# Optimization experiments

Hardware: AMD Instinct MI355X
Metric: run time of the kernel (lower is better)

The kernel has to match this reference:

```python
import jax, jax.numpy as jnp
import numpy as np

N, E, F_IN, F_OUT = 16384, 4096, 128, 128
EPS = 1e-6


def setup_inputs() -> dict:
    key = jax.random.key(0)
    k1, k2, k3 = jax.random.split(key, 3)
    H = (jax.random.uniform(k1, (N, E)) < 0.05).astype(jnp.float32)
    x = jax.random.normal(k2, (N, F_IN), dtype=jnp.float32)
    W = jax.random.normal(k3, (F_IN, F_OUT), dtype=jnp.float32) * 0.05
    return {"x": x, "H": H, "W": W}


def reference(x, H, W):
    # D_v^{-1} H D_e^{-1} H^T x W, computed without materializing the NxN
    # adjacency: diagonal matmuls become row/col broadcast scaling, and the
    # GEMM chain is reordered right-to-left (same math, associativity).
    d_e_inv = 1.0 / (H.sum(axis=0) + EPS)   # [E]
    d_v_inv = 1.0 / (H.sum(axis=1) + EPS)   # [N]
    xw = x @ W                               # [N, F_out]
    edge_msg = H.T @ xw                      # [E, F_out] gather onto edges
    edge_msg = d_e_inv[:, None] * edge_msg   # D_e^{-1}
    node_msg = H @ edge_msg                  # [N, F_out] scatter back to nodes
    return d_v_inv[:, None] * node_msg       # D_v^{-1}
```

## Files before the change

### kernel.cpp

```cpp
#include <hip/hip_runtime.h>
#include <stdint.h>

#define N_NODES 16384
#define N_EDGES 4096
#define FDIM    128
#define EPSF    1e-6f

typedef __attribute__((ext_vector_type(8))) short short8;
typedef __attribute__((ext_vector_type(4))) float f32x4;
typedef unsigned long long ull;

__device__ __forceinline__ unsigned short f2bf(float f) {
    uint32_t u = __float_as_uint(f);
    return (unsigned short)((u + 0x7FFFu + ((u >> 16) & 1u)) >> 16);
}
__device__ __forceinline__ short8 as_s8(uint4 v) {
    union { uint4 a; short8 b; } u; u.a = v; return u.b;
}

__device__ __forceinline__ short8 expand8(uint32_t half, int bitoff) {
    uint32_t b8 = (half >> bitoff) & 0xFFu;
    uint32_t lo = ((b8 & 0xFu) * 0x00204081u) & 0x01010101u;
    uint32_t hi = ((b8 >> 4) * 0x00204081u) & 0x01010101u;
    union { short8 v; uint32_t u[4]; } a;
#if __has_builtin(__builtin_amdgcn_perm)
    a.u[0] = __builtin_amdgcn_perm(0u, lo, 0x04010400u) * 0x3F80u;
    a.u[1] = __builtin_amdgcn_perm(0u, lo, 0x04030402u) * 0x3F80u;
    a.u[2] = __builtin_amdgcn_perm(0u, hi, 0x04010400u) * 0x3F80u;
    a.u[3] = __builtin_amdgcn_perm(0u, hi, 0x04030402u) * 0x3F80u;
#else
    a.u[0] = ((lo & 1u)         | ((lo >> 8) & 1u) << 16) * 0x3F80u;
    a.u[1] = (((lo >> 16) & 1u) | ((lo >> 24) & 1u) << 16) * 0x3F80u;
    a.u[2] = ((hi & 1u)         | ((hi >> 8) & 1u) << 16) * 0x3F80u;
    a.u[3] = (((hi >> 16) & 1u) | ((hi >> 24) & 1u) << 16) * 0x3F80u;
#endif
    return a.v;
}

__device__ __forceinline__ ull bit_transpose64(ull q, int lane) {
    const ull M32 = 0xFFFFFFFF00000000ull, M16 = 0xFFFF0000FFFF0000ull,
              M8 = 0xFF00FF00FF00FF00ull, M4 = 0xF0F0F0F0F0F0F0F0ull,
              M2 = 0xCCCCCCCCCCCCCCCCull, M1 = 0xAAAAAAAAAAAAAAAAull;
#define TSTEP(d, Md) { ull tv = __shfl_xor(q, d, 64); \
    q = ((lane & d) == 0) ? ((q & ~Md) | ((tv << d) & Md)) \
                          : ((q & Md) | ((tv >> d) & ~Md)); }
    TSTEP(32, M32) TSTEP(16, M16) TSTEP(8, M8) TSTEP(4, M4) TSTEP(2, M2) TSTEP(1, M1)
#undef TSTEP
    return q;
}

__global__ __launch_bounds__(256) void k_bitpack(const float* __restrict__ H,
        ull* __restrict__ bitsNE, float* __restrict__ dvinv) {
    int w = threadIdx.x >> 6, lane = threadIdx.x & 63;
    int n = blockIdx.x * 4 + w;
    const float4* hr = (const float4*)(H + (size_t)n * N_EDGES);
    ull* out = bitsNE + (size_t)n * (N_EDGES / 64);
    int cnt = 0;
    for (int c4 = 0; c4 < N_EDGES / 256; ++c4) {
        float4 v = hr[c4 * 64 + lane];
        ull b0 = __ballot(v.x > 0.5f);
        ull b1 = __ballot(v.y > 0.5f);
        ull b2 = __ballot(v.z > 0.5f);
        ull b3 = __ballot(v.w > 0.5f);
        cnt += __popcll(b0) + __popcll(b1) + __popcll(b2) + __popcll(b3);
        if (lane == 0) {
            #pragma unroll
            for (int q = 0; q < 4; ++q) {
                ull wq = ((b0 >> (16 * q)) & 0xFFFFull)
                       | (((b1 >> (16 * q)) & 0xFFFFull) << 16)
                       | (((b2 >> (16 * q)) & 0xFFFFull) << 32)
                       | (((b3 >> (16 * q)) & 0xFFFFull) << 48);
                out[c4 * 4 + q] = wq;
            }
        }
    }
    if (lane == 0) dvinv[n] = 1.0f / ((float)cnt + EPSF);
}

__global__ __launch_bounds__(256) void k_transpose_bf(const ull* __restrict__ bitsNE,
        ull* __restrict__ bitsEN) {
    int w = threadIdx.x >> 6, lane = threadIdx.x & 63;
    int wid = blockIdx.x * 4 + w;
    int nt = wid >> 3, etg = wid & 7;
    int pl = 4 * (lane & 15) + (lane >> 4);
    const ull* src = bitsNE + (size_t)(nt * 64 + pl) * (N_EDGES / 64);
    #pragma unroll
    for (int i = 0; i < 8; ++i) {
        int et = etg * 8 + i;
        ull q = src[et];
        q = bit_transpose64(q, lane);
        bitsEN[(size_t)(et * 64 + pl) * (N_NODES / 64) + nt] = q;
    }
}

__global__ __launch_bounds__(256) void k_edeg(const ull* __restrict__ bitsEN,
        float* __restrict__ deinv) {
    int w = threadIdx.x >> 6, lane = threadIdx.x & 63;
    int e = blockIdx.x * 4 + w;
    const ull* r = bitsEN + (size_t)e * (N_NODES / 64);
    int s = __popcll(r[lane]) + __popcll(r[lane + 64]) + __popcll(r[lane + 128]) + __popcll(r[lane + 192]);
    for (int o = 32; o; o >>= 1) s += __shfl_xor(s, o);
    if (lane == 0) deinv[e] = 1.0f / ((float)s + EPSF);
}

__global__ __launch_bounds__(256) void k_xw(const float* __restrict__ x, const float* __restrict__ W,
        unsigned short* __restrict__ xwTp) {
    __shared__ __attribute__((aligned(16))) unsigned short ldsWT[128 * 136];
    __shared__ __attribute__((aligned(16))) unsigned short ldsT[128 * 72];
    int t = threadIdx.x, lane = t & 63, w = t >> 6;
    int r16 = lane & 15, klane = lane >> 4;
    for (int i = 0; i < 64; ++i) {
        int idx = i * 256 + t;
        int k = idx >> 7, f = idx & 127;
        ldsWT[f * 136 + k] = f2bf(W[idx]);
    }
    __syncthreads();
    int nbase = blockIdx.x * 64;
    int row = nbase + w * 16 + r16;
    const float4* xr4 = (const float4*)(x + (size_t)row * FDIM);
    f32x4 acc[8] = {};
    for (int kb = 0; kb < 128; kb += 32) {
        float4 u0 = xr4[(kb >> 2) + klane * 2];
        float4 u1 = xr4[(kb >> 2) + klane * 2 + 1];
        union { short8 v; unsigned short u[8]; } a;
        a.u[0] = f2bf(u0.x); a.u[1] = f2bf(u0.y); a.u[2] = f2bf(u0.z); a.u[3] = f2bf(u0.w);
        a.u[4] = f2bf(u1.x); a.u[5] = f2bf(u1.y); a.u[6] = f2bf(u1.z); a.u[7] = f2bf(u1.w);
        #pragma unroll
        for (int fb = 0; fb < 8; ++fb) {
            short8 b = *(const short8*)&ldsWT[(fb * 16 + r16) * 136 + kb + klane * 8];
            acc[fb] = __builtin_amdgcn_mfma_f32_16x16x32_bf16(a.v, b, acc[fb], 0, 0, 0);
        }
    }
    #pragma unroll
    for (int fb = 0; fb < 8; ++fb)
        #pragma unroll
        for (int r = 0; r < 4; ++r)
            ldsT[(fb * 16 + r16) * 72 + 16 * r + w * 4 + klane] = f2bf(acc[fb][r]);
    __syncthreads();
    int f = t >> 1, part = t & 1;
    #pragma unroll
    for (int j = 0; j < 4; ++j)
        *(uint4*)&xwTp[(size_t)f * N_NODES + nbase + part * 32 + j * 8] =
            *(const uint4*)&ldsT[f * 72 + part * 32 + j * 8];
}

#define LOADP(Q0, Q1, BUF, p) do { \
    Q0 = brow0[(p)]; Q1 = brow1[(p)]; \
    const unsigned short* _src = bcol + (size_t)(p) * 64; \
    _Pragma("unroll") \
    for (int _fb = 0; _fb < 4; ++_fb) { \
        BUF[_fb * 2]     = *(const uint4*)(_src + _fb * fbstride); \
        BUF[_fb * 2 + 1] = *(const uint4*)(_src + _fb * fbstride + 32); \
    } } while (0)

#define COMPUTEP(Q0, Q1, BUF) do { \
    _Pragma("unroll") \
    for (int _s2 = 0; _s2 < 2; ++_s2) { \
        uint32_t _h0 = (uint32_t)(_s2 == 0 ? (Q0) : ((Q0) >> 32)); \
        uint32_t _h1 = (uint32_t)(_s2 == 0 ? (Q1) : ((Q1) >> 32)); \
        short8 _a0 = expand8(_h0, bitoff); \
        short8 _a1 = expand8(_h1, bitoff); \
        _Pragma("unroll") \
        for (int _f = 0; _f < 4; ++_f) { \
            short8 _b = as_s8(BUF[_f * 2 + _s2]); \
            acc[0][_f] = __builtin_amdgcn_mfma_f32_16x16x32_bf16(_a0, _b, acc[0][_f], 0, 0, 0); \
            acc[1][_f] = __builtin_amdgcn_mfma_f32_16x16x32_bf16(_a1, _b, acc[1][_f], 0, 0, 0); \
        } } } while (0)

template<bool FINAL>
__global__ __launch_bounds__(256, 2) void k_gemm_gen(
        const ull* __restrict__ bits, int krows,
        const unsigned short* __restrict__ BT, int K,
        float* __restrict__ Cout, const float* __restrict__ rowScale,
        int M, int npairs) {
    int t = threadIdx.x, lane = t & 63, w = t >> 6;
    int r16 = lane & 15, klane = lane >> 4;
    int bitoff = klane * 8;
    int wm = w >> 1, wf = w & 1;
    int mbase = blockIdx.x * 64 + wm * 32;
    int kq0 = blockIdx.z * npairs;
    const ull* brow0 = bits + (size_t)(mbase + r16) * krows + kq0;
    const ull* brow1 = brow0 + (size_t)16 * krows;
    const unsigned short* bcol = BT + (size_t)(wf * 64 + r16) * K + (size_t)kq0 * 64 + klane * 8;
    const size_t fbstride = (size_t)16 * K;
    f32x4 acc[2][4] = {};
    ull qA0, qA1, qB0, qB1;
    uint4 bufA[8], bufB[8];
    LOADP(qA0, qA1, bufA, 0);
    for (int p = 0; p < npairs; p += 2) {
        LOADP(qB0, qB1, bufB, p + 1);
        COMPUTEP(qA0, qA1, bufA);
        if (p + 2 < npairs) LOADP(qA0, qA1, bufA, p + 2);
        COMPUTEP(qB0, qB1, bufB);
    }
    #pragma unroll
    for (int fr = 0; fr < 2; ++fr)
        #pragma unroll
        for (int fb = 0; fb < 4; ++fb)
            #pragma unroll
            for (int r = 0; r < 4; ++r) {
                int row = mbase + fr * 16 + klane * 4 + r;
                int col = wf * 64 + fb * 16 + r16;
                float v = acc[fr][fb][r];
                if (FINAL)
                    Cout[(size_t)row * FDIM + col] = rowScale[row] * v;
                else
                    Cout[(size_t)blockIdx.z * M * FDIM + (size_t)row * FDIM + col] = v;
            }
}

__global__ __launch_bounds__(256) void k_reduce_scale_T(const float* __restrict__ partials,
        const float* __restrict__ deinv, unsigned short* __restrict__ emTp, int S) {
    __shared__ float lds[64 * 129];
    int t = threadIdx.x;
    int e0 = blockIdx.x * 64;
    for (int i = 0; i < 32; ++i) {
        int idx = i * 256 + t;
        int e_l = idx >> 7, f = idx & 127;
        float s = 0.f;
        for (int z = 0; z < S; ++z)
            s += partials[(size_t)z * N_EDGES * FDIM + (size_t)(e0 + e_l) * FDIM + f];
        lds[e_l * 129 + f] = s * deinv[e0 + e_l];
    }
    __syncthreads();
    for (int i = 0; i < 32; ++i) {
        int idx = i * 256 + t;
        int f = idx >> 6, j = idx & 63;
        int pj = 4 * (j & 15) + (j >> 4);
        emTp[(size_t)f * N_EDGES + e0 + j] = f2bf(lds[pj * 129 + f]);
    }
}

__global__ __launch_bounds__(256) void k_finalN(const float* __restrict__ partN,
        const float* __restrict__ dvinv, float* __restrict__ out) {
    const float4* pa = (const float4*)partN;
    const float4* pb = (const float4*)(partN + (size_t)N_NODES * FDIM);
    float4* o4 = (float4*)out;
    int t = threadIdx.x;
    #pragma unroll
    for (int i = 0; i < 4; ++i) {
        int idx = blockIdx.x * 1024 + i * 256 + t;
        float4 a = pa[idx], b = pb[idx];
        float s = dvinv[idx >> 5];
        o4[idx] = make_float4((a.x + b.x) * s, (a.y + b.y) * s,
                              (a.z + b.z) * s, (a.w + b.w) * s);
    }
}

extern "C" void kernel_launch(void* const* d_in, const int* in_sizes, int n_in,
                              void* d_out, int out_size, void* d_ws, size_t ws_size,
                              hipStream_t stream) {
    const float* x = (const float*)d_in[0];
    const float* H = (const float*)d_in[1];
    const float* W = (const float*)d_in[2];
    float* out = (float*)d_out;
    char* ws = (char*)d_ws;

    ull* bitsNE = (ull*)(ws);
    ull* bitsEN = (ull*)(ws + (8u << 20));
    unsigned short* xwTp = (unsigned short*)(ws + (16u << 20));
    unsigned short* emTp = (unsigned short*)(ws + (20u << 20));
    float* dvinv = (float*)(ws + (21u << 20));
    float* deinv = (float*)(ws + (21u << 20) + 65536);
    float* partE = (float*)(ws + (22u << 20));
    float* partN = (float*)(ws + (38u << 20));

    int SE = 8;
    while (SE > 1 && (22u << 20) + (size_t)SE * N_EDGES * FDIM * 4 > ws_size) SE >>= 1;
    bool sn2 = ws_size >= ((38u << 20) + (size_t)2 * N_NODES * FDIM * 4);

    hipLaunchKernelGGL(k_bitpack, dim3(4096), dim3(256), 0, stream, H, bitsNE, dvinv);
    hipLaunchKernelGGL(k_transpose_bf, dim3(512), dim3(256), 0, stream, bitsNE, bitsEN);
    hipLaunchKernelGGL(k_edeg, dim3(1024), dim3(256), 0, stream, bitsEN, deinv);
    hipLaunchKernelGGL(k_xw, dim3(256), dim3(256), 0, stream, x, W, xwTp);
    hipLaunchKernelGGL((k_gemm_gen<false>), dim3(64, 1, SE), dim3(256), 0, stream,
                       bitsEN, N_NODES / 64, xwTp, N_NODES, partE, (const float*)nullptr,
                       N_EDGES, (N_NODES / 64) / SE);
    hipLaunchKernelGGL(k_reduce_scale_T, dim3(64), dim3(256), 0, stream, partE, deinv, emTp, SE);
    if (sn2) {
        hipLaunchKernelGGL((k_gemm_gen<false>), dim3(256, 1, 2), dim3(256), 0, stream,
                           bitsNE, N_EDGES / 64, emTp, N_EDGES, partN, (const float*)nullptr,
                           N_NODES, (N_EDGES / 64) / 2);
        hipLaunchKernelGGL(k_finalN, dim3(512), dim3(256), 0, stream, partN, dvinv, out);
    } else {
        hipLaunchKernelGGL((k_gemm_gen<true>), dim3(256, 1, 1), dim3(256), 0, stream,
                           bitsNE, N_EDGES / 64, emTp, N_EDGES, out, dvinv,
                           N_NODES, N_EDGES / 64);
    }
}
```

Baseline: 302.2 us.

## Triple-buffer GEMM loads with fixed K-split, drop node-side split and final reduce

The bit-packed MFMA GEMM now uses a compile-time pair count of 64 and a three-stage rotating register buffer, replacing the two-stage prefetch and keeping more loads in flight. The edge-side GEMM moves from a split of up to 8 to a fixed split of 4. The node-side GEMM runs unsplit and applies D_v^{-1} inline, so k_finalN and the partN buffer are gone. The triple buffer raises register pressure, and the minimum-blocks launch bound is removed, which may lower occupancy. The node GEMM also has half as many blocks in flight as before.

```diff
diff --git a/kernel.cpp b/kernel.cpp
--- a/kernel.cpp
+++ b/kernel.cpp
@@ -5,6 +5,7 @@
 #define N_EDGES 4096
 #define FDIM    128
 #define EPSF    1e-6f
+#define NPAIRS  64
 
 typedef __attribute__((ext_vector_type(8))) short short8;
 typedef __attribute__((ext_vector_type(4))) float f32x4;
@@ -168,31 +169,35 @@
         } } } while (0)
 
 template<bool FINAL>
-__global__ __launch_bounds__(256, 2) void k_gemm_gen(
+__global__ __launch_bounds__(256) void k_gemm_gen(
         const ull* __restrict__ bits, int krows,
         const unsigned short* __restrict__ BT, int K,
-        float* __restrict__ Cout, const float* __restrict__ rowScale,
-        int M, int npairs) {
+        float* __restrict__ Cout, const float* __restrict__ rowScale, int M) {
     int t = threadIdx.x, lane = t & 63, w = t >> 6;
     int r16 = lane & 15, klane = lane >> 4;
     int bitoff = klane * 8;
     int wm = w >> 1, wf = w & 1;
     int mbase = blockIdx.x * 64 + wm * 32;
-    int kq0 = blockIdx.z * npairs;
+    int kq0 = blockIdx.z * NPAIRS;
     const ull* brow0 = bits + (size_t)(mbase + r16) * krows + kq0;
     const ull* brow1 = brow0 + (size_t)16 * krows;
     const unsigned short* bcol = BT + (size_t)(wf * 64 + r16) * K + (size_t)kq0 * 64 + klane * 8;
     const size_t fbstride = (size_t)16 * K;
     f32x4 acc[2][4] = {};
-    ull qA0, qA1, qB0, qB1;
-    uint4 bufA[8], bufB[8];
+    ull qA0, qA1, qB0, qB1, qC0, qC1;
+    uint4 bufA[8], bufB[8], bufC[8];
     LOADP(qA0, qA1, bufA, 0);
-    for (int p = 0; p < npairs; p += 2) {
-        LOADP(qB0, qB1, bufB, p + 1);
-        COMPUTEP(qA0, qA1, bufA);
-        if (p + 2 < npairs) LOADP(qA0, qA1, bufA, p + 2);
-        COMPUTEP(qB0, qB1, bufB);
-    }
+    LOADP(qB0, qB1, bufB, 1);
+    LOADP(qC0, qC1, bufC, 2);
+    for (int p = 0; p <= NPAIRS - 7; p += 3) {
+        COMPUTEP(qA0, qA1, bufA); LOADP(qA0, qA1, bufA, p + 3);
+        COMPUTEP(qB0, qB1, bufB); LOADP(qB0, qB1, bufB, p + 4);
+        COMPUTEP(qC0, qC1, bufC); LOADP(qC0, qC1, bufC, p + 5);
+    }
+    COMPUTEP(qA0, qA1, bufA); LOADP(qA0, qA1, bufA, NPAIRS - 1);
+    COMPUTEP(qB0, qB1, bufB);
+    COMPUTEP(qC0, qC1, bufC);
+    COMPUTEP(qA0, qA1, bufA);
     #pragma unroll
     for (int fr = 0; fr < 2; ++fr)
         #pragma unroll
@@ -231,22 +236,6 @@
     }
 }
 
-__global__ __launch_bounds__(256) void k_finalN(const float* __restrict__ partN,
-        const float* __restrict__ dvinv, float* __restrict__ out) {
-    const float4* pa = (const float4*)partN;
-    const float4* pb = (const float4*)(partN + (size_t)N_NODES * FDIM);
-    float4* o4 = (float4*)out;
-    int t = threadIdx.x;
-    #pragma unroll
-    for (int i = 0; i < 4; ++i) {
-        int idx = blockIdx.x * 1024 + i * 256 + t;
-        float4 a = pa[idx], b = pb[idx];
-        float s = dvinv[idx >> 5];
-        o4[idx] = make_float4((a.x + b.x) * s, (a.y + b.y) * s,
-                              (a.z + b.z) * s, (a.w + b.w) * s);
-    }
-}
-
 extern "C" void kernel_launch(void* const* d_in, const int* in_sizes, int n_in,
                               void* d_out, int out_size, void* d_ws, size_t ws_size,
                               hipStream_t stream) {
@@ -263,28 +252,16 @@
     float* dvinv = (float*)(ws + (21u << 20));
     float* deinv = (float*)(ws + (21u << 20) + 65536);
     float* partE = (float*)(ws + (22u << 20));
-    float* partN = (float*)(ws + (38u << 20));
-
-    int SE = 8;
-    while (SE > 1 && (22u << 20) + (size_t)SE * N_EDGES * FDIM * 4 > ws_size) SE >>= 1;
-    bool sn2 = ws_size >= ((38u << 20) + (size_t)2 * N_NODES * FDIM * 4);
 
     hipLaunchKernelGGL(k_bitpack, dim3(4096), dim3(256), 0, stream, H, bitsNE, dvinv);
     hipLaunchKernelGGL(k_transpose_bf, dim3(512), dim3(256), 0, stream, bitsNE, bitsEN);
     hipLaunchKernelGGL(k_edeg, dim3(1024), dim3(256), 0, stream, bitsEN, deinv);
     hipLaunchKernelGGL(k_xw, dim3(256), dim3(256), 0, stream, x, W, xwTp);
-    hipLaunchKernelGGL((k_gemm_gen<false>), dim3(64, 1, SE), dim3(256), 0, stream,
+    hipLaunchKernelGGL((k_gemm_gen<false>), dim3(64, 1, 4), dim3(256), 0, stream,
                        bitsEN, N_NODES / 64, xwTp, N_NODES, partE, (const float*)nullptr,
-                       N_EDGES, (N_NODES / 64) / SE);
-    hipLaunchKernelGGL(k_reduce_scale_T, dim3(64), dim3(256), 0, stream, partE, deinv, emTp, SE);
-    if (sn2) {
-        hipLaunchKernelGGL((k_gemm_gen<false>), dim3(256, 1, 2), dim3(256), 0, stream,
-                           bitsNE, N_EDGES / 64, emTp, N_EDGES, partN, (const float*)nullptr,
-                           N_NODES, (N_EDGES / 64) / 2);
-        hipLaunchKernelGGL(k_finalN, dim3(512), dim3(256), 0, stream, partN, dvinv, out);
-    } else {
-        hipLaunchKernelGGL((k_gemm_gen<true>), dim3(256, 1, 1), dim3(256), 0, stream,
-                           bitsNE, N_EDGES / 64, emTp, N_EDGES, out, dvinv,
-                           N_NODES, N_EDGES / 64);
-    }
-}
+                       N_EDGES);
+    hipLaunchKernelGGL(k_reduce_scale_T, dim3(64), dim3(256), 0, stream, partE, deinv, emTp, 4);
+    hipLaunchKernelGGL((k_gemm_gen<true>), dim3(256, 1, 1), dim3(256), 0, stream,
+                       bitsNE, N_EDGES / 64, emTp, N_EDGES, out, dvinv,
+                       N_NODES);
+}
```

Measured after the change: 250.3 us, median of 2. 17.2% less time.
